# Kernel tuning notes

Measured on AMD Instinct MI355X. Metric: run time of the kernel, lower is better.

The kernel has to match this reference:

```python
import jax, jax.numpy as jnp
import numpy as np

# Architecture constants (from RUMamba.__init__ hard-coded Mamba2 config)
D_MODEL = 512
D_STATE = 128
D_CONV = 4
EXPAND = 4
HEADDIM = 32
D_INNER = EXPAND * D_MODEL            # 2048
NHEADS = D_INNER // HEADDIM           # 64
CONV_DIM = D_INNER + 2 * D_STATE      # 2304 (ngroups=1)
D_IN_PROJ = 2 * D_INNER + 2 * D_STATE + NHEADS  # 4416
NUM_CLASS = 2513
BATCH = 4
SEQ = 16


def setup_inputs() -> dict:
    key = jax.random.key(0)
    ks = jax.random.split(key, 8)
    inputs = jax.random.normal(ks[0], (BATCH, SEQ, D_MODEL), jnp.float32)
    in_proj_w = jax.random.normal(ks[1], (D_IN_PROJ, D_MODEL), jnp.float32) * 0.02
    conv_w = jax.random.normal(ks[2], (CONV_DIM, D_CONV), jnp.float32) * 0.2
    conv_b = jnp.zeros((CONV_DIM,), jnp.float32)
    # dt_bias initialized so softplus(dt_bias) ~ U(0.001, 0.1), as in Mamba2
    dt = jax.random.uniform(ks[3], (NHEADS,), jnp.float32, 0.001, 0.1)
    dt_bias = dt + jnp.log(-jnp.expm1(-dt))
    A_log = jnp.log(jax.random.uniform(ks[4], (NHEADS,), jnp.float32, 1.0, 16.0))
    cls_w = jax.random.normal(ks[5], (NUM_CLASS, HEADDIM * D_STATE), jnp.float32) * 0.02
    cls_b = jnp.zeros((NUM_CLASS,), jnp.float32)
    return {"inputs": inputs, "in_proj_w": in_proj_w, "conv_w": conv_w,
            "conv_b": conv_b, "dt_bias": dt_bias, "A_log": A_log,
            "cls_w": cls_w, "cls_b": cls_b}


def reference(inputs, in_proj_w, conv_w, conv_b, dt_bias, A_log, cls_w, cls_b):
    # inputs: (B, S, D) -> (S, B, D) as in forward's permute(1,0,2)
    seq = jnp.transpose(inputs, (1, 0, 2))
    S, B, _ = seq.shape

    # Shared in_proj for both rolling and unrolling (same Mamba math on inputs[t]).
    zxbcdt = jnp.einsum('sbd,ed->sbe', seq, in_proj_w)        # (S,B,4416)
    xBC_raw = zxbcdt[..., D_INNER:D_INNER + CONV_DIM]          # (S,B,2304)
    dt = jax.nn.softplus(zxbcdt[..., -NHEADS:] + dt_bias)      # (S,B,H)
    A = -jnp.exp(A_log)                                        # (H,)
    dA = jnp.exp(dt * A)                                       # (S,B,H)

    # --- Rolling pass: one length-1 Mamba call per timestep, SSM state carried,
    # conv state NOT carried -> causal conv on a length-1 seq uses only last tap.
    xBC_r = jax.nn.silu(xBC_raw * conv_w[:, -1] + conv_b)      # (S,B,2304)
    x_r = xBC_r[..., :D_INNER].reshape(S, B, NHEADS, HEADDIM)  # (S,B,H,P)
    B_r = xBC_r[..., D_INNER:D_INNER + D_STATE]                # (S,B,N)
    dBx = dt[..., None, None] * B_r[:, :, None, None, :] * x_r[..., None]  # (S,B,H,P,N)

    def roll_step(h, inp):
        dA_t, dBx_t = inp
        h = dA_t[..., None, None] * h + dBx_t
        return h, h

    h0 = jnp.zeros((B, NHEADS, HEADDIM, D_STATE), seq.dtype)
    _, states = jax.lax.scan(roll_step, h0, (dA, dBx))         # (S,B,H,P,N)

    # --- Unrolling pass: for each t, feed inputs[t] repeated (S - t + 1) times
    # starting from states[t]. Constant input => conv output only depends on
    # min(step, d_conv-1) via cumulative sums of reversed conv taps.
    cw = jnp.cumsum(conv_w[:, ::-1], axis=1)                   # (2304,4)
    t_idx = jnp.arange(S)

    def unroll_step(h, k):
        w_k = cw[:, jnp.minimum(k, D_CONV - 1)]                # (2304,)
        xBC_k = jax.nn.silu(xBC_raw * w_k + conv_b)            # (S,B,2304)
        x_k = xBC_k[..., :D_INNER].reshape(S, B, NHEADS, HEADDIM)
        B_k = xBC_k[..., D_INNER:D_INNER + D_STATE]
        h_new = dA[..., None, None] * h + \
            dt[..., None, None] * B_k[:, :, None, None, :] * x_k[..., None]
        active = (k <= S - t_idx)[:, None, None, None, None]   # length S - t + 1
        return jnp.where(active, h_new, h), None

    h_fin, _ = jax.lax.scan(unroll_step, states, jnp.arange(S + 1))  # (S,B,H,P,N)

    # Head-reduce to headdim*d_state = 4096 features, classify.
    feats = jnp.mean(h_fin, axis=2).reshape(S, B, HEADDIM * D_STATE)
    feats = jnp.transpose(feats, (1, 0, 2))                    # (B,S,4096)
    y = feats @ cls_w.T + cls_b                                # (B,S,num_class)
    return y
```

## Files before the change

kernel.cpp:

```cpp
#include <hip/hip_runtime.h>
#include <math.h>

#define S_LEN    16
#define NTOK     64
#define DMODEL   512
#define XB_COLS  2176
#define ZX_COLS  2240
#define NCLASS   2513
#define FEATDIM  4096
#define PD_STRIDE 2516

typedef float f4v __attribute__((ext_vector_type(4)));

__global__ __launch_bounds__(256) void k_fpart(const float* __restrict__ X,
                                               const float* __restrict__ W,
                                               float* __restrict__ partF) {
    const int tid = threadIdx.x;
    const int kf  = blockIdx.y;
    const int jb  = blockIdx.x * 64;
    const int k0  = kf * 64;

    __shared__ float A[64][64];
    __shared__ float B[64][64];

    {
        const int t  = tid >> 2;
        const int kq = tid & 3;
        const int xrow = (t & 3) * 16 + (t >> 2);
        const int e = (jb + t < XB_COLS) ? (2048 + jb + t) : (2176 + jb + t);
#pragma unroll
        for (int q = 0; q < 4; ++q) {
            const int kk = kq * 16 + q * 4;
            const float4 va = *reinterpret_cast<const float4*>(
                X + (size_t)xrow * DMODEL + k0 + kk);
            A[kk + 0][t] = va.x; A[kk + 1][t] = va.y;
            A[kk + 2][t] = va.z; A[kk + 3][t] = va.w;
            const float4 vb = *reinterpret_cast<const float4*>(
                W + (size_t)e * DMODEL + k0 + kk);
            B[kk + 0][t] = vb.x; B[kk + 1][t] = vb.y;
            B[kk + 2][t] = vb.z; B[kk + 3][t] = vb.w;
        }
    }
    __syncthreads();

    const int ti = tid >> 4;
    const int ci = tid & 15;
    float acc[4][4] = {{0.f}};
#pragma unroll 4
    for (int k = 0; k < 64; ++k) {
        const f4v a = *reinterpret_cast<const f4v*>(&A[k][ti * 4]);
        const f4v b = *reinterpret_cast<const f4v*>(&B[k][ci * 4]);
#pragma unroll
        for (int j = 0; j < 4; ++j)
#pragma unroll
            for (int l = 0; l < 4; ++l)
                acc[j][l] += a[j] * b[l];
    }
#pragma unroll
    for (int l = 0; l < 4; ++l) {
        f4v s; s[0] = acc[0][l]; s[1] = acc[1][l]; s[2] = acc[2][l]; s[3] = acc[3][l];
        *reinterpret_cast<f4v*>(
            partF + ((size_t)kf * ZX_COLS + jb + ci * 4 + l) * 64 + ti * 4) = s;
    }
}

__global__ __launch_bounds__(256) void k_fepi(const float* __restrict__ partF, int KF,
                                              const float* __restrict__ conv_w,
                                              const float* __restrict__ conv_b,
                                              const float* __restrict__ dt_bias,
                                              const float* __restrict__ A_log,
                                              float* __restrict__ u,
                                              float* __restrict__ aArr,
                                              float* __restrict__ dArr) {
    const int lane = threadIdx.x & 63;
    const int j    = blockIdx.x * 4 + (threadIdx.x >> 6);
    float acc = 0.f;
    for (int kf = 0; kf < KF; ++kf)
        acc += partF[((size_t)kf * ZX_COLS + j) * 64 + lane];

    if (j < XB_COLS) {
        const float4 cwv = *reinterpret_cast<const float4*>(conv_w + j * 4);
        const float cb = conv_b[j];
        float wk[4];
        wk[0] = cwv.w;
        wk[1] = wk[0] + cwv.z;
        wk[2] = wk[1] + cwv.y;
        wk[3] = wk[2] + cwv.x;
#pragma unroll
        for (int k = 0; k < 4; ++k) {
            const float v = acc * wk[k] + cb;
            u[((size_t)k * NTOK + lane) * XB_COLS + j] = v / (1.f + expf(-v));
        }
    } else {
        const int h = j - XB_COLS;
        const float x = acc + dt_bias[h];
        const float d = (x > 20.f) ? x : log1pf(expf(x));
        dArr[lane * 64 + h] = d;
        aArr[lane * 64 + h] = expf(-d * expf(A_log[h]));
    }
}

__global__ __launch_bounds__(256) void k_feats(const float* __restrict__ u,
                                               const float* __restrict__ aArr,
                                               const float* __restrict__ dArr,
                                               float* __restrict__ feats) {
    const int t = blockIdx.x >> 2;
    const int b = blockIdx.x & 3;
    const int tid = threadIdx.x;
    const int K = 16 - t;
    const int nvec = t + 5;

    __shared__ float q[16][64];
    __shared__ float cu[4][64];
    __shared__ float WV[20][32];
    __shared__ float Bv[20][128];

    if (tid < 64) {
        const int h = tid;
        const int mt = t * 4 + b;
        const float a   = aArr[mt * 64 + h];
        const float dtv = dArr[mt * 64 + h];
        float p = 1.f;
        float c3 = 0.f, c2 = 0.f, c1 = 0.f, c0 = 0.f, cs = 0.f;
        for (int j = 0; j <= K + 1; ++j) {
            if (j <= K - 3) c3 += p;
            if (j == K - 2) c2 = p;
            if (j == K - 1) c1 = p;
            if (j == K)     c0 = p;
            if (j == K + 1) cs = p;
            p *= a;
        }
        cu[0][h] = dtv * c0;
        cu[1][h] = dtv * c1;
        cu[2][h] = dtv * c2;
        cu[3][h] = dtv * c3;
        float prod = 1.f;
        for (int s = t; s >= 0; --s) {
            const int ms = s * 4 + b;
            q[s][h] = cs * prod * dArr[ms * 64 + h];
            prod *= aArr[ms * 64 + h];
        }
    }
    __syncthreads();

    {
        const int i = tid & 31;
        const int vs = tid >> 5;
        for (int v = vs; v < nvec; v += 8) {
            float acc = 0.f;
            if (v <= t) {
                const float* base = u + (size_t)(v * 4 + b) * XB_COLS;
                for (int h = 0; h < 64; ++h) acc += q[v][h] * base[h * 32 + i];
            } else {
                const int kk = v - t - 1;
                const float* base = u + ((size_t)kk * NTOK + t * 4 + b) * XB_COLS;
                for (int h = 0; h < 64; ++h) acc += cu[kk][h] * base[h * 32 + i];
            }
            WV[v][i] = acc;
        }
    }
    for (int x = tid; x < nvec * 128; x += 256) {
        const int v = x >> 7, n = x & 127;
        size_t src;
        if (v <= t) src = (size_t)(v * 4 + b) * XB_COLS + 2048 + n;
        else        src = ((size_t)(v - t - 1) * NTOK + t * 4 + b) * XB_COLS + 2048 + n;
        Bv[v][n] = u[src];
    }
    __syncthreads();

    {
        const int i  = tid >> 3;
        const int n0 = (tid & 7) * 16;
        const int r  = b * 16 + t;
        float acc[16];
#pragma unroll
        for (int nn = 0; nn < 16; ++nn) acc[nn] = 0.f;
        for (int v = 0; v < nvec; ++v) {
            const float wvv = WV[v][i];
#pragma unroll
            for (int nn = 0; nn < 16; ++nn) acc[nn] += wvv * Bv[v][n0 + nn];
        }
        float* dst = feats + (size_t)r * FEATDIM + i * 128 + n0;
#pragma unroll
        for (int qq = 0; qq < 4; ++qq) {
            float4 v4;
            v4.x = acc[qq * 4 + 0] * (1.f / 64.f);
            v4.y = acc[qq * 4 + 1] * (1.f / 64.f);
            v4.z = acc[qq * 4 + 2] * (1.f / 64.f);
            v4.w = acc[qq * 4 + 3] * (1.f / 64.f);
            *reinterpret_cast<float4*>(dst + qq * 4) = v4;
        }
    }
}

__global__ __launch_bounds__(256) void k_cls(const float* __restrict__ feats,
                                             const float* __restrict__ Wc,
                                             float* __restrict__ partialD) {
    const int tid   = threadIdx.x;
    const int lane  = tid & 63;
    const int wv    = tid >> 6;
    const int ks    = blockIdx.y;
    const int cls0  = blockIdx.x * 64;
    const int chunk = FEATDIM / gridDim.y;
    const int nsub  = chunk / 64;

    __shared__ float lds[12288];
    float (*A)[64] = (float(*)[64])lds;
    float (*B)[64] = (float(*)[64])(lds + 4096);

    const int ti = lane >> 3;
    const int ci = lane & 7;

    float acc[8][8] = {{0.f}};

    for (int st = 0; st < nsub; ++st) {
        const int k0 = ks * chunk + st * 64;
        __syncthreads();
        {
            const int t  = tid >> 2;
            const int kq = tid & 3;
            int cr = cls0 + t; if (cr > NCLASS - 1) cr = NCLASS - 1;
#pragma unroll
            for (int q = 0; q < 4; ++q) {
                const int kk = kq * 16 + q * 4;
                const float4 va = *reinterpret_cast<const float4*>(
                    feats + (size_t)t * FEATDIM + k0 + kk);
                A[kk + 0][t] = va.x; A[kk + 1][t] = va.y;
                A[kk + 2][t] = va.z; A[kk + 3][t] = va.w;
                const float4 vb = *reinterpret_cast<const float4*>(
                    Wc + (size_t)cr * FEATDIM + k0 + kk);
                B[kk + 0][t] = vb.x; B[kk + 1][t] = vb.y;
                B[kk + 2][t] = vb.z; B[kk + 3][t] = vb.w;
            }
        }
        __syncthreads();

#pragma unroll
        for (int k = 0; k < 16; ++k) {
            const int kk = wv * 16 + k;
            const f4v a0 = *reinterpret_cast<const f4v*>(&A[kk][ti * 4]);
            const f4v a1 = *reinterpret_cast<const f4v*>(&A[kk][32 + ti * 4]);
            const f4v b0 = *reinterpret_cast<const f4v*>(&B[kk][ci * 4]);
            const f4v b1 = *reinterpret_cast<const f4v*>(&B[kk][32 + ci * 4]);
#pragma unroll
            for (int j = 0; j < 4; ++j) {
#pragma unroll
                for (int l = 0; l < 4; ++l) {
                    acc[j][l]         += a0[j] * b0[l];
                    acc[j][l + 4]     += a0[j] * b1[l];
                    acc[j + 4][l]     += a1[j] * b0[l];
                    acc[j + 4][l + 4] += a1[j] * b1[l];
                }
            }
        }
    }

    __syncthreads();
    if (wv > 0) {
        const int w = wv - 1;
#pragma unroll
        for (int i = 0; i < 64; ++i)
            lds[w * 4096 + i * 64 + lane] = acc[i >> 3][i & 7];
    }
    __syncthreads();
    if (wv == 0) {
#pragma unroll
        for (int i = 0; i < 64; ++i)
            acc[i >> 3][i & 7] += lds[i * 64 + lane]
                                + lds[4096 + i * 64 + lane]
                                + lds[8192 + i * 64 + lane];

        const size_t obase = (size_t)ks * (NTOK * PD_STRIDE);
#pragma unroll
        for (int ta = 0; ta < 2; ++ta) {
#pragma unroll
            for (int j = 0; j < 4; ++j) {
                const int row = ta * 32 + ti * 4 + j;
#pragma unroll
                for (int cb = 0; cb < 2; ++cb) {
                    const int c = cls0 + cb * 32 + ci * 4;
                    f4v s;
#pragma unroll
                    for (int l = 0; l < 4; ++l) s[l] = acc[ta * 4 + j][cb * 4 + l];
                    float* dst = partialD + obase + (size_t)row * PD_STRIDE + c;
                    if (c + 3 < NCLASS) {
                        *reinterpret_cast<f4v*>(dst) = s;
                    } else {
#pragma unroll
                        for (int l = 0; l < 4; ++l)
                            if (c + l < NCLASS) dst[l] = s[l];
                    }
                }
            }
        }
    }
}

__global__ void k_out(const float* __restrict__ partialD, const float* __restrict__ cls_b,
                      float* __restrict__ out, int NP) {
    const int bx = blockIdx.x;
    const int r  = bx / 10;
    const int c  = (bx % 10) * 256 + threadIdx.x;
    if (c >= NCLASS) return;
    float s = cls_b[c];
    for (int p = 0; p < NP; ++p)
        s += partialD[(size_t)p * (NTOK * PD_STRIDE) + (size_t)r * PD_STRIDE + c];
    out[(size_t)r * NCLASS + c] = s;
}

extern "C" void kernel_launch(void* const* d_in, const int* in_sizes, int n_in,
                              void* d_out, int out_size, void* d_ws, size_t ws_size,
                              hipStream_t stream) {
    const float* inputs  = (const float*)d_in[0];
    const float* in_proj = (const float*)d_in[1];
    const float* conv_w  = (const float*)d_in[2];
    const float* conv_b  = (const float*)d_in[3];
    const float* dt_bias = (const float*)d_in[4];
    const float* A_log   = (const float*)d_in[5];
    const float* cls_w   = (const float*)d_in[6];
    const float* cls_b   = (const float*)d_in[7];
    float* out = (float*)d_out;

    float* ws = (float*)d_ws;
    float* aArr    = ws;
    float* dArr    = ws + 4096;
    float* feats   = ws + 8192;
    float* scr     = ws + 270336;
    float* u       = scr;
    float* partF   = scr + 557056;
    float* partialD = scr;

    int KC;
    if (ws_size >= 11386880u) KC = 16;
    else                      KC = 8;

    k_fpart <<<dim3(35, 8), 256, 0, stream>>>(inputs, in_proj, partF);
    k_fepi  <<<560, 256, 0, stream>>>(partF, 8, conv_w, conv_b, dt_bias, A_log,
                                      u, aArr, dArr);
    k_feats <<<64, 256, 0, stream>>>(u, aArr, dArr, feats);
    k_cls   <<<dim3(40, KC), 256, 0, stream>>>(feats, cls_w, partialD);
    k_out   <<<640, 256, 0, stream>>>(partialD, cls_b, out, KC);
}
```

Baseline: 64.55 us.

## Transpose partF layout, coalesce epilogue, and prefetch classifier tiles with padded LDS

Partial products from the in_proj GEMM are now stored token-major with contiguous columns, so the epilogue kernel reads and writes coalesced rows using a flat thread index. The classifier GEMM now loads the next K-slab into registers while the current slab is being computed (register double-buffering). It also transposes 4x4 blocks into padded shared memory rows of stride 68, which cuts bank conflicts and replaces scalar LDS stores with vector stores. In exchange the kernel uses more registers, and the epilogue grid indexing must match the new launch configuration.

Measured after the change: 61.30 us. 1.05x faster.

```diff
diff --git a/kernel.cpp b/kernel.cpp
--- a/kernel.cpp
+++ b/kernel.cpp
@@ -9,6 +9,7 @@
 #define NCLASS   2513
 #define FEATDIM  4096
 #define PD_STRIDE 2516
+#define APAD     68
 
 typedef float f4v __attribute__((ext_vector_type(4)));
 
@@ -57,10 +58,11 @@
                 acc[j][l] += a[j] * b[l];
     }
 #pragma unroll
-    for (int l = 0; l < 4; ++l) {
-        f4v s; s[0] = acc[0][l]; s[1] = acc[1][l]; s[2] = acc[2][l]; s[3] = acc[3][l];
+    for (int jj = 0; jj < 4; ++jj) {
+        f4v s; s[0] = acc[jj][0]; s[1] = acc[jj][1];
+               s[2] = acc[jj][2]; s[3] = acc[jj][3];
         *reinterpret_cast<f4v*>(
-            partF + ((size_t)kf * ZX_COLS + jb + ci * 4 + l) * 64 + ti * 4) = s;
+            partF + ((size_t)kf * NTOK + ti * 4 + jj) * ZX_COLS + jb + ci * 4) = s;
     }
 }
 
@@ -72,11 +74,12 @@
                                               float* __restrict__ u,
                                               float* __restrict__ aArr,
                                               float* __restrict__ dArr) {
-    const int lane = threadIdx.x & 63;
-    const int j    = blockIdx.x * 4 + (threadIdx.x >> 6);
+    const int idx = blockIdx.x * 256 + threadIdx.x;
+    const int m = idx / ZX_COLS;
+    const int j = idx - m * ZX_COLS;
     float acc = 0.f;
     for (int kf = 0; kf < KF; ++kf)
-        acc += partF[((size_t)kf * ZX_COLS + j) * 64 + lane];
+        acc += partF[((size_t)kf * NTOK + m) * ZX_COLS + j];
 
     if (j < XB_COLS) {
         const float4 cwv = *reinterpret_cast<const float4*>(conv_w + j * 4);
@@ -89,14 +92,14 @@
 #pragma unroll
         for (int k = 0; k < 4; ++k) {
             const float v = acc * wk[k] + cb;
-            u[((size_t)k * NTOK + lane) * XB_COLS + j] = v / (1.f + expf(-v));
+            u[((size_t)k * NTOK + m) * XB_COLS + j] = v / (1.f + expf(-v));
         }
     } else {
         const int h = j - XB_COLS;
         const float x = acc + dt_bias[h];
         const float d = (x > 20.f) ? x : log1pf(expf(x));
-        dArr[lane * 64 + h] = d;
-        aArr[lane * 64 + h] = expf(-d * expf(A_log[h]));
+        dArr[m * 64 + h] = d;
+        aArr[m * 64 + h] = expf(-d * expf(A_log[h]));
     }
 }
 
@@ -205,43 +208,61 @@
     const int nsub  = chunk / 64;
 
     __shared__ float lds[12288];
-    float (*A)[64] = (float(*)[64])lds;
-    float (*B)[64] = (float(*)[64])(lds + 4096);
+    float* A = lds;
+    float* B = lds + 64 * APAD;
+
+    const int rq = tid >> 4;
+    const int kq = tid & 15;
+    int crow[4];
+#pragma unroll
+    for (int r = 0; r < 4; ++r) {
+        int cr = cls0 + rq * 4 + r; if (cr > NCLASS - 1) cr = NCLASS - 1;
+        crow[r] = cr;
+    }
 
     const int ti = lane >> 3;
     const int ci = lane & 7;
 
+    float4 pa[4], pb[4];
+#define LOADREGS(ST)                                                      \
+    do {                                                                  \
+        const int k0_ = ks * chunk + (ST) * 64 + kq * 4;                  \
+        _Pragma("unroll")                                                 \
+        for (int r = 0; r < 4; ++r) {                                     \
+            pa[r] = *reinterpret_cast<const float4*>(                     \
+                feats + (size_t)(rq * 4 + r) * FEATDIM + k0_);            \
+            pb[r] = *reinterpret_cast<const float4*>(                     \
+                Wc + (size_t)crow[r] * FEATDIM + k0_);                    \
+        }                                                                 \
+    } while (0)
+
     float acc[8][8] = {{0.f}};
 
+    LOADREGS(0);
     for (int st = 0; st < nsub; ++st) {
-        const int k0 = ks * chunk + st * 64;
         __syncthreads();
         {
-            const int t  = tid >> 2;
-            const int kq = tid & 3;
-            int cr = cls0 + t; if (cr > NCLASS - 1) cr = NCLASS - 1;
-#pragma unroll
-            for (int q = 0; q < 4; ++q) {
-                const int kk = kq * 16 + q * 4;
-                const float4 va = *reinterpret_cast<const float4*>(
-                    feats + (size_t)t * FEATDIM + k0 + kk);
-                A[kk + 0][t] = va.x; A[kk + 1][t] = va.y;
-                A[kk + 2][t] = va.z; A[kk + 3][t] = va.w;
-                const float4 vb = *reinterpret_cast<const float4*>(
-                    Wc + (size_t)cr * FEATDIM + k0 + kk);
-                B[kk + 0][t] = vb.x; B[kk + 1][t] = vb.y;
-                B[kk + 2][t] = vb.z; B[kk + 3][t] = vb.w;
+#pragma unroll
+            for (int s = 0; s < 4; ++s) {
+                const int kk = kq * 4 + s;
+                f4v wa; wa[0] = (&pa[0].x)[s]; wa[1] = (&pa[1].x)[s];
+                        wa[2] = (&pa[2].x)[s]; wa[3] = (&pa[3].x)[s];
+                *reinterpret_cast<f4v*>(&A[kk * APAD + rq * 4]) = wa;
+                f4v wb; wb[0] = (&pb[0].x)[s]; wb[1] = (&pb[1].x)[s];
+                        wb[2] = (&pb[2].x)[s]; wb[3] = (&pb[3].x)[s];
+                *reinterpret_cast<f4v*>(&B[kk * APAD + rq * 4]) = wb;
             }
         }
+        if (st + 1 < nsub) LOADREGS(st + 1);
         __syncthreads();
 
 #pragma unroll
         for (int k = 0; k < 16; ++k) {
             const int kk = wv * 16 + k;
-            const f4v a0 = *reinterpret_cast<const f4v*>(&A[kk][ti * 4]);
-            const f4v a1 = *reinterpret_cast<const f4v*>(&A[kk][32 + ti * 4]);
-            const f4v b0 = *reinterpret_cast<const f4v*>(&B[kk][ci * 4]);
-            const f4v b1 = *reinterpret_cast<const f4v*>(&B[kk][32 + ci * 4]);
+            const f4v a0 = *reinterpret_cast<const f4v*>(&A[kk * APAD + ti * 4]);
+            const f4v a1 = *reinterpret_cast<const f4v*>(&A[kk * APAD + 32 + ti * 4]);
+            const f4v b0 = *reinterpret_cast<const f4v*>(&B[kk * APAD + ci * 4]);
+            const f4v b1 = *reinterpret_cast<const f4v*>(&B[kk * APAD + 32 + ci * 4]);
 #pragma unroll
             for (int j = 0; j < 4; ++j) {
 #pragma unroll
@@ -254,6 +275,7 @@
             }
         }
     }
+#undef LOADREGS
 
     __syncthreads();
     if (wv > 0) {
```
